# Performance work log

Measured on AMD Instinct MI355X. Metric: run time of the kernel, lower is better.

Reference implementation:

```python
import jax, jax.numpy as jnp
import numpy as np

NUM_HEADS = 16
D_MODEL = 1024
DEPTH = D_MODEL // NUM_HEADS


def rope_sincos(seq_len, depth):
    # standard RoPE: inv_freq over even dims, sin/cos tiled to full depth
    inv_freq = 1.0 / (10000.0 ** (jnp.arange(0, depth, 2, dtype=jnp.float32) / depth))
    ang = jnp.arange(seq_len, dtype=jnp.float32)[:, None] * inv_freq[None, :]  # [S, depth/2]
    sin = jnp.concatenate([jnp.sin(ang), jnp.sin(ang)], axis=-1)  # [S, depth]
    cos = jnp.concatenate([jnp.cos(ang), jnp.cos(ang)], axis=-1)
    return sin, cos


def apply_rope(x, sin, cos):
    # x: [B,H,S,depth]; rotate-half formulation
    half = x.shape[-1] // 2
    x1, x2 = x[..., :half], x[..., half:]
    rot = jnp.concatenate([-x2, x1], axis=-1)
    return x * cos + rot * sin


def setup_inputs() -> dict:
    key = jax.random.key(0)
    ks = jax.random.split(key, 5)
    s = 1.0 / np.sqrt(D_MODEL)
    return {
        "x": jax.random.normal(ks[0], (2, 2048, D_MODEL), dtype=jnp.float32),
        "wq": jax.random.normal(ks[1], (D_MODEL, D_MODEL), dtype=jnp.float32) * s,
        "bq": jnp.zeros((D_MODEL,), jnp.float32),
        "wk": jax.random.normal(ks[2], (D_MODEL, D_MODEL), dtype=jnp.float32) * s,
        "bk": jnp.zeros((D_MODEL,), jnp.float32),
        "wv": jax.random.normal(ks[3], (D_MODEL, D_MODEL), dtype=jnp.float32) * s,
        "bv": jnp.zeros((D_MODEL,), jnp.float32),
        "wo": jax.random.normal(ks[4], (D_MODEL, D_MODEL), dtype=jnp.float32) * s,
        "bo": jnp.zeros((D_MODEL,), jnp.float32),
    }


def reference(x, wq, bq, wk, bk, wv, bv, wo, bo):
    B, S, _ = x.shape

    def split_heads(t):  # [B,S,D] -> [B,H,S,depth]
        return t.reshape(B, S, NUM_HEADS, DEPTH).transpose(0, 2, 1, 3)

    Q = split_heads(x @ wq + bq)
    K = split_heads(x @ wk + bk)
    V = split_heads(x @ wv + bv)

    sin, cos = rope_sincos(S, DEPTH)  # [S, depth], broadcasts over B,H
    Q = apply_rope(Q, sin, cos)
    K = apply_rope(K, sin, cos)

    scores = jnp.einsum("bhqd,bhkd->bhqk", Q, K) / jnp.sqrt(jnp.float32(DEPTH))
    weights = jax.nn.softmax(scores, axis=-1)
    out = jnp.einsum("bhqk,bhkd->bhqd", weights, V)
    out = out.transpose(0, 2, 1, 3).reshape(B, S, D_MODEL)
    return out @ wo + bo
```

## Files before the change

kernel.cpp:

```cpp
#include <hip/hip_runtime.h>

#define DM 1024
#define SEQ 2048
#define NH 16
#define DH 64
#define BATCH 2

typedef _Float16 half_t;
typedef _Float16 half8 __attribute__((ext_vector_type(8)));
typedef _Float16 half4 __attribute__((ext_vector_type(4)));
typedef __fp16 f16x2 __attribute__((ext_vector_type(2)));
typedef unsigned u32x2 __attribute__((ext_vector_type(2)));
typedef unsigned u32x4 __attribute__((ext_vector_type(4)));
typedef float f32x4 __attribute__((ext_vector_type(4)));

__device__ __forceinline__ f32x4 mfma16(half8 a, half8 b, f32x4 c) {
  return __builtin_amdgcn_mfma_f32_16x16x32_f16(a, b, c, 0, 0, 0);
}

__device__ __forceinline__ void gl2lds16(const half_t* g, half_t* l) {
  __builtin_amdgcn_global_load_lds((const __attribute__((address_space(1))) void*)g,
                                   (__attribute__((address_space(3))) void*)l, 16, 0, 0);
}


__global__ void cvt_x_kernel(const float* __restrict__ x, half_t* __restrict__ xh) {
  int i = (blockIdx.x * 256 + threadIdx.x) * 4;
  float4 v = *(const float4*)(x + i);
  half4 h = { (half_t)v.x, (half_t)v.y, (half_t)v.z, (half_t)v.w };
  *(half4*)(xh + i) = h;
}

__global__ void wtrans_kernel(const float* __restrict__ w0, const float* __restrict__ w1,
                              const float* __restrict__ w2, const float* __restrict__ w3,
                              half_t* __restrict__ o0, half_t* __restrict__ o1,
                              half_t* __restrict__ o2, half_t* __restrict__ o3) {
  __shared__ float tile[32][33];
  const float* w = (blockIdx.z == 0) ? w0 : (blockIdx.z == 1) ? w1 : (blockIdx.z == 2) ? w2 : w3;
  half_t* o = (blockIdx.z == 0) ? o0 : (blockIdx.z == 1) ? o1 : (blockIdx.z == 2) ? o2 : o3;
  int tx = threadIdx.x, ty0 = threadIdx.y;
  int bx = blockIdx.x * 32, by = blockIdx.y * 32;
#pragma unroll
  for (int i = 0; i < 4; i++) {
    int ty = ty0 + i * 8;
    tile[ty][tx] = w[(size_t)(by + ty) * DM + bx + tx];
  }
  __syncthreads();
#pragma unroll
  for (int i = 0; i < 4; i++) {
    int ty = ty0 + i * 8;
    o[(size_t)(bx + ty) * DM + by + tx] = (half_t)tile[tx][ty];
  }
}

__global__ void ropetab_kernel(float* __restrict__ st, float* __restrict__ ct) {
  int idx = blockIdx.x * 256 + threadIdx.x;
  int s = idx >> 5, i = idx & 31;
  float freq = exp2f(-(float)i * (13.287712379549449f / 32.0f));
  float ang = (float)s * freq;
  st[idx] = sinf(ang);
  ct[idx] = cosf(ang);
}


__global__ __launch_bounds__(256)
void qkv_kernel(const half_t* __restrict__ xh,
                const half_t* __restrict__ wtq, const half_t* __restrict__ wtk,
                const half_t* __restrict__ wtv,
                const float* __restrict__ bq, const float* __restrict__ bk,
                const float* __restrict__ bv,
                const float* __restrict__ st, const float* __restrict__ ctab,
                half_t* __restrict__ Qh, half_t* __restrict__ Kh, half_t* __restrict__ Vt) {
  const int tid = threadIdx.x;
  const int wid = tid >> 6, lane = tid & 63;
  const int l16 = lane & 15, quad = lane >> 4;
  const int m0 = blockIdx.y * 128, n0 = blockIdx.x * 128;
  const int g = blockIdx.z;
  const half_t* wt = (g == 0) ? wtq : (g == 1) ? wtk : wtv;
  const float* bias = (g == 0) ? bq : (g == 1) ? bk : bv;
  __shared__ __align__(16) half_t As[128 * 32];
  __shared__ __align__(16) half_t Bs[128 * 32];
  __shared__ __align__(16) half_t vtile[4][64 * 72];
  f32x4 acc[4][4] = {};
  const int wrow = (wid >> 1) * 64, wcol = (wid & 1) * 64;

  const int ar0 = tid >> 2,          ab0 = (tid & 3) ^ ((ar0 >> 1) & 3);
  const int ar1 = (tid + 256) >> 2,  ab1 = (tid & 3) ^ ((ar1 >> 1) & 3);
  const int swz = (l16 >> 1) & 3;

  for (int k0 = 0; k0 < DM; k0 += 32) {
    __syncthreads();
    gl2lds16(&xh[(size_t)(m0 + ar0) * DM + k0 + ab0 * 8], &As[tid * 8]);
    gl2lds16(&xh[(size_t)(m0 + ar1) * DM + k0 + ab1 * 8], &As[(tid + 256) * 8]);
    gl2lds16(&wt[(size_t)(n0 + ar0) * DM + k0 + ab0 * 8], &Bs[tid * 8]);
    gl2lds16(&wt[(size_t)(n0 + ar1) * DM + k0 + ab1 * 8], &Bs[(tid + 256) * 8]);
    __syncthreads();
    half8 a[4], b[4];
#pragma unroll
    for (int rt = 0; rt < 4; rt++)
      a[rt] = *(const half8*)&As[((wrow + rt * 16 + l16) * 4 + (quad ^ swz)) * 8];
#pragma unroll
    for (int ct = 0; ct < 4; ct++)
      b[ct] = *(const half8*)&Bs[((wcol + ct * 16 + l16) * 4 + (quad ^ swz)) * 8];
#pragma unroll
    for (int rt = 0; rt < 4; rt++)
#pragma unroll
      for (int ct = 0; ct < 4; ct++)
        acc[rt][ct] = mfma16(a[rt], b[ct], acc[rt][ct]);
  }

  const int h = (n0 + wcol) >> 6;
  const float qscale = 0.125f * 1.44269504089f;
  float bv4[4];
#pragma unroll
  for (int ct = 0; ct < 4; ct++) bv4[ct] = bias[n0 + wcol + ct * 16 + l16];

  if (g == 2) {
    half_t* vt = vtile[wid];
#pragma unroll
    for (int rt = 0; rt < 4; rt++)
#pragma unroll
      for (int ct = 0; ct < 4; ct++) {
        half4 hv;
#pragma unroll
        for (int r = 0; r < 4; r++) hv[r] = (half_t)(acc[rt][ct][r] + bv4[ct]);
        *(half4*)&vt[(ct * 16 + l16) * 72 + rt * 16 + quad * 4] = hv;
      }
    const int sb = m0 + wrow;
    const int bb = sb >> 11, s0 = sb & 2047;
    half_t* dstv = Vt + (size_t)(bb * NH + h) * DH * SEQ;
#pragma unroll
    for (int i = 0; i < 8; i++) {
      int d = i * 8 + (lane >> 3), soff = (lane & 7) * 8;
      half8 v = *(const half8*)&vt[d * 72 + soff];
      *(half8*)&dstv[(size_t)d * SEQ + s0 + soff] = v;
    }
  } else {
    half_t* dst = (g == 0) ? Qh : Kh;
#pragma unroll
    for (int rt = 0; rt < 4; rt++) {
#pragma unroll
      for (int r = 0; r < 4; r++) {
        int m = m0 + wrow + rt * 16 + quad * 4 + r;
        int bb = m >> 11, s = m & 2047;
        float v0 = acc[rt][0][r] + bv4[0];
        float v1 = acc[rt][1][r] + bv4[1];
        float v2 = acc[rt][2][r] + bv4[2];
        float v3 = acc[rt][3][r] + bv4[3];
        float sn0 = st[s * 32 + l16], cs0 = ctab[s * 32 + l16];
        float sn1 = st[s * 32 + 16 + l16], cs1 = ctab[s * 32 + 16 + l16];
        float o0 = v0 * cs0 - v2 * sn0;
        float o1 = v1 * cs1 - v3 * sn1;
        float o2 = v2 * cs0 + v0 * sn0;
        float o3 = v3 * cs1 + v1 * sn1;
        if (g == 0) { o0 *= qscale; o1 *= qscale; o2 *= qscale; o3 *= qscale; }
        size_t base = ((size_t)(bb * NH + h) * SEQ + s) * DH;
        dst[base + l16]      = (half_t)o0;
        dst[base + 16 + l16] = (half_t)o1;
        dst[base + 32 + l16] = (half_t)o2;
        dst[base + 48 + l16] = (half_t)o3;
      }
    }
  }
}


__global__ __launch_bounds__(256)
void attn_kernel(const half_t* __restrict__ Qh, const half_t* __restrict__ Kh,
                 const half_t* __restrict__ Vt, half_t* __restrict__ AO) {
  const int tid = threadIdx.x;
  const int wid = tid >> 6, lane = tid & 63;
  const int l16 = lane & 15, quad = lane >> 4;
  const int bh = blockIdx.y;
  const int bb = bh >> 4, h = bh & 15;
  const int q0 = blockIdx.x * 128 + wid * 32;
  const half_t* Q = Qh + (size_t)bh * SEQ * DH;
  const half_t* K = Kh + (size_t)bh * SEQ * DH;
  const half_t* V = Vt + (size_t)bh * DH * SEQ;
  __shared__ __align__(16) half_t Ks[2][64 * 64];
  __shared__ __align__(16) half_t Vs[2][64 * 64];
  __shared__ __align__(16) half_t pbuf[4][32 * 72];
  half_t* myp = pbuf[wid];

  const int r0 = tid >> 3,         c0 = (tid & 7) ^ (r0 & 7);
  const int r1 = (tid + 256) >> 3, c1 = (tid & 7) ^ (r1 & 7);
  const int sw0 = ((quad ^ (l16 & 7)) * 8);
  const int sw1 = (((quad + 4) ^ (l16 & 7)) * 8);

  const half_t* gK0 = &K[(size_t)r0 * DH + c0 * 8];
  const half_t* gK1 = &K[(size_t)r1 * DH + c1 * 8];
  const half_t* gV0 = &V[(size_t)r0 * SEQ + c0 * 8];
  const half_t* gV1 = &V[(size_t)r1 * SEQ + c1 * 8];

  half8 aqA[2], aqB[2];
#pragma unroll
  for (int rt = 0; rt < 2; rt++) {
    aqA[rt] = *(const half8*)&Q[(size_t)(q0 + rt * 16 + l16) * DH + quad * 8];
    aqB[rt] = *(const half8*)&Q[(size_t)(q0 + rt * 16 + l16) * DH + 32 + quad * 8];
  }

  f32x4 o[2][4] = {};
  f32x4 vsum[2] = {};
  const f32x4 cinit = {-12.f, -12.f, -12.f, -12.f};

  gl2lds16(gK0, &Ks[0][tid * 8]);
  gl2lds16(gK1, &Ks[0][(tid + 256) * 8]);
  gl2lds16(gV0, &Vs[0][tid * 8]);
  gl2lds16(gV1, &Vs[0][(tid + 256) * 8]);
  __syncthreads();

  int cur = 0;
  for (int kb0 = 0; kb0 < SEQ; kb0 += 64) {
    const bool pf = (kb0 + 64 < SEQ);
    u32x4 rk0, rk1, rv0, rv1;
    if (pf) {
      const int kb = kb0 + 64;
      rk0 = *(const u32x4*)(gK0 + (size_t)kb * DH);
      rk1 = *(const u32x4*)(gK1 + (size_t)kb * DH);
      rv0 = *(const u32x4*)(gV0 + kb);
      rv1 = *(const u32x4*)(gV1 + kb);
    }
    const half_t* ksrc = Ks[cur];
    const half_t* vsrc = Vs[cur];

    f32x4 z[2][4];
    __builtin_amdgcn_s_setprio(1);
#pragma unroll
    for (int kt = 0; kt < 4; kt++) {
      const half_t* krow = &ksrc[(kt * 16 + l16) * 64];
      half8 b0 = *(const half8*)&krow[sw0];
      half8 b1 = *(const half8*)&krow[sw1];
#pragma unroll
      for (int rt = 0; rt < 2; rt++) {
        f32x4 zz = cinit;
        zz = mfma16(b0, aqA[rt], zz);
        zz = mfma16(b1, aqB[rt], zz);
        z[rt][kt] = zz;
      }
    }
    __builtin_amdgcn_s_setprio(0);

#pragma unroll
    for (int rt = 0; rt < 2; rt++)
#pragma unroll
      for (int kt = 0; kt < 4; kt++) {
        f32x4 p;
#pragma unroll
        for (int r = 0; r < 4; r++) p[r] = __builtin_amdgcn_exp2f(z[rt][kt][r]);
        vsum[rt] += p;
        f16x2 lo = __builtin_amdgcn_cvt_pkrtz(p[0], p[1]);
        f16x2 hi = __builtin_amdgcn_cvt_pkrtz(p[2], p[3]);
        u32x2 w = { __builtin_bit_cast(unsigned, lo), __builtin_bit_cast(unsigned, hi) };
        *(u32x2*)&myp[(rt * 16 + l16) * 72 + kt * 16 + quad * 4] = w;
      }

    half8 ap0[2], ap1[2];
#pragma unroll
    for (int rt = 0; rt < 2; rt++) {
      ap0[rt] = *(const half8*)&myp[(rt * 16 + l16) * 72 + quad * 8];
      ap1[rt] = *(const half8*)&myp[(rt * 16 + l16) * 72 + 32 + quad * 8];
    }
    __builtin_amdgcn_s_setprio(1);
#pragma unroll
    for (int dt = 0; dt < 4; dt++) {
      const half_t* vrow = &vsrc[(dt * 16 + l16) * 64];
      half8 bv0 = *(const half8*)&vrow[sw0];
      half8 bv1 = *(const half8*)&vrow[sw1];
#pragma unroll
      for (int rt = 0; rt < 2; rt++) {
        o[rt][dt] = mfma16(ap0[rt], bv0, o[rt][dt]);
        o[rt][dt] = mfma16(ap1[rt], bv1, o[rt][dt]);
      }
    }
    __builtin_amdgcn_s_setprio(0);

    if (pf) {
      const int nxt = cur ^ 1;
      *(u32x4*)&Ks[nxt][tid * 8] = rk0;
      *(u32x4*)&Ks[nxt][(tid + 256) * 8] = rk1;
      *(u32x4*)&Vs[nxt][tid * 8] = rv0;
      *(u32x4*)&Vs[nxt][(tid + 256) * 8] = rv1;
    }
    __syncthreads();
    cur ^= 1;
  }

  float linv[2][4];
#pragma unroll
  for (int rt = 0; rt < 2; rt++) {
    float s = (vsum[rt][0] + vsum[rt][1]) + (vsum[rt][2] + vsum[rt][3]);
    s += __shfl_xor(s, 16);
    s += __shfl_xor(s, 32);
#pragma unroll
    for (int r = 0; r < 4; r++) linv[rt][r] = 1.f / __shfl(s, quad * 4 + r);
  }
#pragma unroll
  for (int rt = 0; rt < 2; rt++)
#pragma unroll
    for (int dt = 0; dt < 4; dt++)
#pragma unroll
      for (int r = 0; r < 4; r++) {
        int srow = q0 + rt * 16 + quad * 4 + r;
        AO[((size_t)bb * SEQ + srow) * DM + h * DH + dt * 16 + l16] =
            (half_t)(o[rt][dt][r] * linv[rt][r]);
      }
}


__global__ __launch_bounds__(256)
void out_kernel(const half_t* __restrict__ AO, const half_t* __restrict__ wto,
                const float* __restrict__ bo, float* __restrict__ out) {
  const int tid = threadIdx.x;
  const int wid = tid >> 6, lane = tid & 63;
  const int l16 = lane & 15, quad = lane >> 4;
  const int m0 = blockIdx.y * 128, n0 = blockIdx.x * 64;
  __shared__ __align__(16) half_t As[128 * 32];
  __shared__ __align__(16) half_t Bs[64 * 32];
  f32x4 acc[4][2] = {};
  const int wrow = (wid >> 1) * 64, wcol = (wid & 1) * 32;

  const int ar0 = tid >> 2,         ab0 = (tid & 3) ^ ((ar0 >> 1) & 3);
  const int ar1 = (tid + 256) >> 2, ab1 = (tid & 3) ^ ((ar1 >> 1) & 3);
  const int swz = (l16 >> 1) & 3;

  for (int k0 = 0; k0 < DM; k0 += 32) {
    __syncthreads();
    gl2lds16(&AO[(size_t)(m0 + ar0) * DM + k0 + ab0 * 8], &As[tid * 8]);
    gl2lds16(&AO[(size_t)(m0 + ar1) * DM + k0 + ab1 * 8], &As[(tid + 256) * 8]);
    gl2lds16(&wto[(size_t)(n0 + ar0) * DM + k0 + ab0 * 8], &Bs[tid * 8]);
    __syncthreads();
    half8 a[4], b[2];
#pragma unroll
    for (int rt = 0; rt < 4; rt++)
      a[rt] = *(const half8*)&As[((wrow + rt * 16 + l16) * 4 + (quad ^ swz)) * 8];
#pragma unroll
    for (int ct = 0; ct < 2; ct++)
      b[ct] = *(const half8*)&Bs[((wcol + ct * 16 + l16) * 4 + (quad ^ swz)) * 8];
#pragma unroll
    for (int rt = 0; rt < 4; rt++)
#pragma unroll
      for (int ct = 0; ct < 2; ct++)
        acc[rt][ct] = mfma16(a[rt], b[ct], acc[rt][ct]);
  }
  float bv2[2];
#pragma unroll
  for (int ct = 0; ct < 2; ct++) bv2[ct] = bo[n0 + wcol + ct * 16 + l16];
#pragma unroll
  for (int rt = 0; rt < 4; rt++)
#pragma unroll
    for (int r = 0; r < 4; r++) {
      int m = m0 + wrow + rt * 16 + quad * 4 + r;
#pragma unroll
      for (int ct = 0; ct < 2; ct++)
        out[(size_t)m * DM + n0 + wcol + ct * 16 + l16] = acc[rt][ct][r] + bv2[ct];
    }
}


extern "C" void kernel_launch(void* const* d_in, const int* in_sizes, int n_in,
                              void* d_out, int out_size, void* d_ws, size_t ws_size,
                              hipStream_t stream) {
  (void)in_sizes; (void)n_in; (void)out_size; (void)ws_size;
  const float* x  = (const float*)d_in[0];
  const float* wq = (const float*)d_in[1];
  const float* bq = (const float*)d_in[2];
  const float* wk = (const float*)d_in[3];
  const float* bk = (const float*)d_in[4];
  const float* wv = (const float*)d_in[5];
  const float* bv = (const float*)d_in[6];
  const float* wo = (const float*)d_in[7];
  const float* bo = (const float*)d_in[8];
  char* ws = (char*)d_ws;
  const size_t MB = 1u << 20;
  half_t* xh  = (half_t*)(ws + 0);
  half_t* AO  = (half_t*)(ws + 0);
  half_t* wtq = (half_t*)(ws + 8 * MB);
  half_t* wtk = (half_t*)(ws + 10 * MB);
  half_t* wtv = (half_t*)(ws + 12 * MB);
  half_t* wto = (half_t*)(ws + 14 * MB);
  float*  st  = (float*)(ws + 16 * MB);
  float*  ctb = (float*)(ws + 16 * MB + 256 * 1024);
  half_t* Qh  = (half_t*)(ws + 17 * MB);
  half_t* Kh  = (half_t*)(ws + 25 * MB);
  half_t* Vt  = (half_t*)(ws + 33 * MB);
  float* out = (float*)d_out;

  cvt_x_kernel<<<4096, 256, 0, stream>>>(x, xh);
  wtrans_kernel<<<dim3(32, 32, 4), dim3(32, 8), 0, stream>>>(wq, wk, wv, wo, wtq, wtk, wtv, wto);
  ropetab_kernel<<<256, 256, 0, stream>>>(st, ctb);
  qkv_kernel<<<dim3(8, 32, 3), 256, 0, stream>>>(xh, wtq, wtk, wtv, bq, bk, bv, st, ctb, Qh, Kh, Vt);
  attn_kernel<<<dim3(16, 32), 256, 0, stream>>>(Qh, Kh, Vt, AO);
  out_kernel<<<dim3(16, 32), 256, 0, stream>>>(AO, wto, bo, out);
}
```

Baseline: 207.5 us.

## Use 512-thread attention blocks sharing K/V tiles and alias QKV shared memory

The attention kernel now runs 8 waves per block, each covering 256 queries of one head, so every K/V tile staged in LDS is reused by twice as many query rows. Each thread does a single cooperative load per tile, and a flat block index interleaves heads across query tiles. The QKV kernel reuses the GEMM staging buffers for the V transpose tile with an XOR swizzle instead of padding, which cuts its LDS footprint. The trade-off is half as many attention blocks (256 instead of 512) and more waves stalled at each barrier.

```diff
diff --git a/kernel.cpp b/kernel.cpp
--- a/kernel.cpp
+++ b/kernel.cpp
@@ -78,9 +78,9 @@
   const int g = blockIdx.z;
   const half_t* wt = (g == 0) ? wtq : (g == 1) ? wtk : wtv;
   const float* bias = (g == 0) ? bq : (g == 1) ? bk : bv;
-  __shared__ __align__(16) half_t As[128 * 32];
-  __shared__ __align__(16) half_t Bs[128 * 32];
-  __shared__ __align__(16) half_t vtile[4][64 * 72];
+  __shared__ __align__(16) char smem[32768];
+  half_t* As = (half_t*)smem;
+  half_t* Bs = (half_t*)(smem + 8192);
   f32x4 acc[4][4] = {};
   const int wrow = (wid >> 1) * 64, wcol = (wid & 1) * 64;
 
@@ -116,7 +116,8 @@
   for (int ct = 0; ct < 4; ct++) bv4[ct] = bias[n0 + wcol + ct * 16 + l16];
 
   if (g == 2) {
-    half_t* vt = vtile[wid];
+    __syncthreads();
+    half_t* vt = (half_t*)(smem + wid * 8192);
 #pragma unroll
     for (int rt = 0; rt < 4; rt++)
 #pragma unroll
@@ -124,16 +125,18 @@
         half4 hv;
 #pragma unroll
         for (int r = 0; r < 4; r++) hv[r] = (half_t)(acc[rt][ct][r] + bv4[ct]);
-        *(half4*)&vt[(ct * 16 + l16) * 72 + rt * 16 + quad * 4] = hv;
+        int row = ct * 16 + l16;
+        int colu = rt * 2 + (quad >> 1);
+        *(half4*)&vt[row * 64 + ((colu ^ (row & 7)) * 8) + (quad & 1) * 4] = hv;
       }
     const int sb = m0 + wrow;
     const int bb = sb >> 11, s0 = sb & 2047;
     half_t* dstv = Vt + (size_t)(bb * NH + h) * DH * SEQ;
 #pragma unroll
     for (int i = 0; i < 8; i++) {
-      int d = i * 8 + (lane >> 3), soff = (lane & 7) * 8;
-      half8 v = *(const half8*)&vt[d * 72 + soff];
-      *(half8*)&dstv[(size_t)d * SEQ + s0 + soff] = v;
+      int d = i * 8 + (lane >> 3), c = lane & 7;
+      half8 v = *(const half8*)&vt[d * 64 + ((c ^ (d & 7)) * 8)];
+      *(half8*)&dstv[(size_t)d * SEQ + s0 + c * 8] = v;
     }
   } else {
     half_t* dst = (g == 0) ? Qh : Kh;
@@ -165,32 +168,30 @@
 }
 
 
-__global__ __launch_bounds__(256)
+__global__ __launch_bounds__(512)
 void attn_kernel(const half_t* __restrict__ Qh, const half_t* __restrict__ Kh,
                  const half_t* __restrict__ Vt, half_t* __restrict__ AO) {
   const int tid = threadIdx.x;
   const int wid = tid >> 6, lane = tid & 63;
   const int l16 = lane & 15, quad = lane >> 4;
-  const int bh = blockIdx.y;
+  const int lid = blockIdx.x;
+  const int bh = lid & 31, qt = lid >> 5;
   const int bb = bh >> 4, h = bh & 15;
-  const int q0 = blockIdx.x * 128 + wid * 32;
+  const int q0 = qt * 256 + wid * 32;
   const half_t* Q = Qh + (size_t)bh * SEQ * DH;
   const half_t* K = Kh + (size_t)bh * SEQ * DH;
   const half_t* V = Vt + (size_t)bh * DH * SEQ;
   __shared__ __align__(16) half_t Ks[2][64 * 64];
   __shared__ __align__(16) half_t Vs[2][64 * 64];
-  __shared__ __align__(16) half_t pbuf[4][32 * 72];
+  __shared__ __align__(16) half_t pbuf[8][32 * 72];
   half_t* myp = pbuf[wid];
 
-  const int r0 = tid >> 3,         c0 = (tid & 7) ^ (r0 & 7);
-  const int r1 = (tid + 256) >> 3, c1 = (tid & 7) ^ (r1 & 7);
+  const int r0 = tid >> 3, c0 = (tid & 7) ^ (r0 & 7);
   const int sw0 = ((quad ^ (l16 & 7)) * 8);
   const int sw1 = (((quad + 4) ^ (l16 & 7)) * 8);
 
   const half_t* gK0 = &K[(size_t)r0 * DH + c0 * 8];
-  const half_t* gK1 = &K[(size_t)r1 * DH + c1 * 8];
   const half_t* gV0 = &V[(size_t)r0 * SEQ + c0 * 8];
-  const half_t* gV1 = &V[(size_t)r1 * SEQ + c1 * 8];
 
   half8 aqA[2], aqB[2];
 #pragma unroll
@@ -204,21 +205,17 @@
   const f32x4 cinit = {-12.f, -12.f, -12.f, -12.f};
 
   gl2lds16(gK0, &Ks[0][tid * 8]);
-  gl2lds16(gK1, &Ks[0][(tid + 256) * 8]);
   gl2lds16(gV0, &Vs[0][tid * 8]);
-  gl2lds16(gV1, &Vs[0][(tid + 256) * 8]);
   __syncthreads();
 
   int cur = 0;
   for (int kb0 = 0; kb0 < SEQ; kb0 += 64) {
     const bool pf = (kb0 + 64 < SEQ);
-    u32x4 rk0, rk1, rv0, rv1;
+    u32x4 rk0, rv0;
     if (pf) {
       const int kb = kb0 + 64;
       rk0 = *(const u32x4*)(gK0 + (size_t)kb * DH);
-      rk1 = *(const u32x4*)(gK1 + (size_t)kb * DH);
       rv0 = *(const u32x4*)(gV0 + kb);
-      rv1 = *(const u32x4*)(gV1 + kb);
     }
     const half_t* ksrc = Ks[cur];
     const half_t* vsrc = Vs[cur];
@@ -277,9 +274,7 @@
     if (pf) {
       const int nxt = cur ^ 1;
       *(u32x4*)&Ks[nxt][tid * 8] = rk0;
-      *(u32x4*)&Ks[nxt][(tid + 256) * 8] = rk1;
       *(u32x4*)&Vs[nxt][tid * 8] = rv0;
-      *(u32x4*)&Vs[nxt][(tid + 256) * 8] = rv1;
     }
     __syncthreads();
     cur ^= 1;
@@ -389,6 +384,6 @@
   wtrans_kernel<<<dim3(32, 32, 4), dim3(32, 8), 0, stream>>>(wq, wk, wv, wo, wtq, wtk, wtv, wto);
   ropetab_kernel<<<256, 256, 0, stream>>>(st, ctb);
   qkv_kernel<<<dim3(8, 32, 3), 256, 0, stream>>>(xh, wtq, wtk, wtv, bq, bk, bv, st, ctb, Qh, Kh, Vt);
-  attn_kernel<<<dim3(16, 32), 256, 0, stream>>>(Qh, Kh, Vt, AO);
+  attn_kernel<<<256, 512, 0, stream>>>(Qh, Kh, Vt, AO);
   out_kernel<<<dim3(16, 32), 256, 0, stream>>>(AO, wto, bo, out);
 }
```

After: 202.1 us. 1.03x faster.
